# Kernel optimization log

Measured on AMD Instinct MI355X. Metric: run time of the kernel, lower is better.

Reference implementation:

```python
import jax, jax.numpy as jnp
import numpy as np

D_MODEL = 1024
NUM_HEADS = 16
D_K = D_MODEL // NUM_HEADS


def setup_inputs() -> dict:
    key = jax.random.key(0)
    ks = jax.random.split(key, 11)
    B, S = 1, 4096
    s = 1.0 / np.sqrt(D_MODEL)
    return {
        "query": jax.random.normal(ks[0], (B, S, D_MODEL), jnp.float32),
        "key": jax.random.normal(ks[1], (B, S, D_MODEL), jnp.float32),
        "value": jax.random.normal(ks[2], (B, S, D_MODEL), jnp.float32),
        "Wq": jax.random.normal(ks[3], (D_MODEL, D_MODEL), jnp.float32) * s,
        "bq": jnp.zeros((D_MODEL,), jnp.float32),
        "Wk": jax.random.normal(ks[4], (D_MODEL, D_MODEL), jnp.float32) * s,
        "bk": jnp.zeros((D_MODEL,), jnp.float32),
        "Wv": jax.random.normal(ks[5], (D_MODEL, D_MODEL), jnp.float32) * s,
        "bv": jnp.zeros((D_MODEL,), jnp.float32),
        "Wo": jax.random.normal(ks[6], (D_MODEL, D_MODEL), jnp.float32) * s,
        "bo": jnp.zeros((D_MODEL,), jnp.float32),
    }


def reference(query, key, value, Wq, bq, Wk, bk, Wv, bv, Wo, bo):
    B, S, _ = query.shape
    # linear projections, split into heads: [B, H, S, d_k]
    def proj(x, W, b):
        y = x @ W.T + b
        return y.reshape(B, -1, NUM_HEADS, D_K).transpose(0, 2, 1, 3)

    q = proj(query, Wq, bq)
    k = proj(key, Wk, bk)
    v = proj(value, Wv, bv)

    scale = D_K ** (-0.5)
    scores = jnp.einsum("bhqd,bhkd->bhqk", q, k) * scale  # [B,H,S,S]
    attn = jax.nn.softmax(scores, axis=-1)
    out = jnp.einsum("bhqk,bhkd->bhqd", attn, v)  # [B,H,S,d_k]
    out = out.transpose(0, 2, 1, 3).reshape(B, -1, NUM_HEADS * D_K)
    return out @ Wo.T + bo
```

## Files before the change

kernel.cpp:

```cpp
#include <hip/hip_runtime.h>

typedef __bf16 bf16;
typedef __bf16 bf16x8 __attribute__((ext_vector_type(8)));
typedef __bf16 bf16x4 __attribute__((ext_vector_type(4)));
typedef float floatx4 __attribute__((ext_vector_type(4)));

#define MFMA(a, b, c) __builtin_amdgcn_mfma_f32_16x16x32_bf16((a), (b), (c), 0, 0, 0)

__device__ inline bf16x8 load8(const bf16* p) { return *(const bf16x8*)(p); }
__device__ inline bf16x4 load4(const bf16* p) { return *(const bf16x4*)(p); }
__device__ inline bf16x8 cat44(bf16x4 a, bf16x4 b) {
    return __builtin_shufflevector(a, b, 0, 1, 2, 3, 4, 5, 6, 7);
}

__device__ inline void store_c(bf16* p, float v) { *p = (bf16)v; }
__device__ inline void store_c(float* p, float v) { *p = v; }

__device__ inline float fast_exp2(float x) {
#if __has_builtin(__builtin_amdgcn_exp2f)
    return __builtin_amdgcn_exp2f(x);
#else
    float r;
    asm("v_exp_f32 %0, %1" : "=v"(r) : "v"(x));
    return r;
#endif
}

__device__ inline float fast_rcp(float x) {
#if __has_builtin(__builtin_amdgcn_rcpf)
    return __builtin_amdgcn_rcpf(x);
#else
    float r;
    asm("v_rcp_f32 %0, %1" : "=v"(r) : "v"(x));
    return r;
#endif
}

__device__ inline void gload_lds(const bf16* g, bf16* l) {
    __builtin_amdgcn_global_load_lds(
        (const __attribute__((address_space(1))) void*)(g),
        (__attribute__((address_space(3))) void*)(l), 16, 0, 0);
}

struct CvtArgs {
    const float* src[7];
    bf16* dst[7];
    int n[7];
};
__global__ __launch_bounds__(256) void cvt_bf16(CvtArgs a) {
    const int t = blockIdx.y;
    const int i = (blockIdx.x * 256 + threadIdx.x) * 8;
    if (i >= a.n[t]) return;
    const float4 u = *(const float4*)(a.src[t] + i);
    const float4 v = *(const float4*)(a.src[t] + i + 4);
    bf16x8 r;
    r[0] = (bf16)u.x; r[1] = (bf16)u.y; r[2] = (bf16)u.z; r[3] = (bf16)u.w;
    r[4] = (bf16)v.x; r[5] = (bf16)v.y; r[6] = (bf16)v.z; r[7] = (bf16)v.w;
    *(bf16x8*)(a.dst[t] + i) = r;
}

template <typename TC>
__device__ inline void gemm_core(const bf16* __restrict__ A, const bf16* __restrict__ W,
                                 const float* __restrict__ bias, TC* __restrict__ C,
                                 bool TR) {
    __shared__ bf16 As[2][128][32];
    __shared__ bf16 Bs[2][128][32];

    const int tid = threadIdx.x;
    const int wv = tid >> 6, lane = tid & 63;
    const int quad = lane >> 4, lo = lane & 15;
    const int wm = wv >> 1, wn = wv & 1;
    const int Ar0 = blockIdx.y * 128, Br0 = blockIdx.x * 128;

    const int srow = lane >> 2, sseg = (lane & 3) ^ (srow & 3);
    const bf16* Ag = A + (size_t)(Ar0 + srow) * 1024 + sseg * 8;
    const bf16* Bg = W + (size_t)(Br0 + srow) * 1024 + sseg * 8;

    auto stage = [&](int buf, int k0) {
#pragma unroll
        for (int c = 2 * wv; c < 2 * wv + 2; c++) {
            gload_lds(Ag + (size_t)c * 16 * 1024 + k0, &As[buf][c * 16][0]);
            gload_lds(Bg + (size_t)c * 16 * 1024 + k0, &Bs[buf][c * 16][0]);
        }
    };

    floatx4 acc[4][4] = {};
    const int rs = (quad ^ (lo & 3)) * 8;

    stage(0, 0);
    for (int k0 = 0; k0 < 1024; k0 += 32) {
        const int buf = (k0 >> 5) & 1;
        __syncthreads();
        if (k0 + 32 < 1024) stage(buf ^ 1, k0 + 32);

        bf16x8 a[4], b[4];
#pragma unroll
        for (int i = 0; i < 4; i++) a[i] = load8(&As[buf][wm * 64 + i * 16 + lo][rs]);
#pragma unroll
        for (int j = 0; j < 4; j++) b[j] = load8(&Bs[buf][wn * 64 + j * 16 + lo][rs]);
#pragma unroll
        for (int i = 0; i < 4; i++)
#pragma unroll
            for (int j = 0; j < 4; j++) acc[i][j] = MFMA(a[i], b[j], acc[i][j]);
    }

#pragma unroll
    for (int i = 0; i < 4; i++) {
#pragma unroll
        for (int j = 0; j < 4; j++) {
#pragma unroll
            for (int r = 0; r < 4; r++) {
                const int m = Ar0 + wm * 64 + i * 16 + quad * 4 + r;
                const int n = Br0 + wn * 64 + j * 16 + lo;
                const float v = acc[i][j][r] + bias[n];
                if (!TR) {
                    store_c(C + (size_t)m * 1024 + n, v);
                } else {
                    store_c(C + (size_t)(n >> 6) * (64 * 4096) + (size_t)(n & 63) * 4096 + m, v);
                }
            }
        }
    }
}

__global__ __launch_bounds__(256) void gemm_qkv(
    const bf16* __restrict__ qb, const bf16* __restrict__ kb, const bf16* __restrict__ vb,
    const bf16* __restrict__ Wq, const bf16* __restrict__ Wk, const bf16* __restrict__ Wv,
    const float* __restrict__ bq, const float* __restrict__ bk, const float* __restrict__ bv,
    bf16* __restrict__ Q, bf16* __restrict__ Kp, bf16* __restrict__ Vt) {
    if (blockIdx.z == 0)
        gemm_core<bf16>(qb, Wq, bq, Q, false);
    else if (blockIdx.z == 1)
        gemm_core<bf16>(kb, Wk, bk, Kp, false);
    else
        gemm_core<bf16>(vb, Wv, bv, Vt, true);
}

__global__ __launch_bounds__(256) void gemm_o(const bf16* __restrict__ O,
                                              const bf16* __restrict__ Wo,
                                              const float* __restrict__ bo,
                                              float* __restrict__ out) {
    gemm_core<float>(O, Wo, bo, out, false);
}

__global__ __launch_bounds__(256) void flash_attn7(const bf16* __restrict__ Q,
                                                   const bf16* __restrict__ Kmat,
                                                   const bf16* __restrict__ Vt,
                                                   bf16* __restrict__ O) {
    __shared__ bf16 Ks[2][64][64];
    __shared__ bf16 Vs[2][64][64];

    const int tid = threadIdx.x;
    const int wv = tid >> 6;
    const int lane = tid & 63;
    const int quad = lane >> 4, lo = lane & 15;
    const int h = blockIdx.x;
    const int qb = blockIdx.y;
    const int DM = 1024;
    const int q0 = qb * 128 + wv * 32;

    bf16x8 aQ[2][2];
#pragma unroll
    for (int qs = 0; qs < 2; qs++) {
        const bf16* qp = Q + (size_t)(q0 + qs * 16 + lo) * DM + h * 64 + quad * 8;
        aQ[qs][0] = load8(qp);
        aQ[qs][1] = load8(qp + 32);
    }

    bf16x8 bOnes;
#pragma unroll
    for (int i = 0; i < 8; i++) bOnes[i] = (bf16)1.0f;

    floatx4 Oacc[2][4] = {};
    floatx4 Lacc[2] = {};

    const int srow = lane >> 3, sseg = (lane & 7) ^ srow;
    const bf16* Kg = Kmat + (size_t)srow * DM + h * 64 + sseg * 8;
    const bf16* Vg = Vt + (size_t)h * 64 * 4096 + (size_t)srow * 4096 + sseg * 8;

    auto stage = [&](int buf, int kb2) {
#pragma unroll
        for (int c = 2 * wv; c < 2 * wv + 2; c++) {
            gload_lds(Kg + (size_t)(kb2 + c * 8) * DM, &Ks[buf][c * 8][0]);
            gload_lds(Vg + (size_t)(c * 8) * 4096 + kb2, &Vs[buf][c * 8][0]);
        }
    };

    const float C_SCALE = 0.18033688011112043f;
    const float C_BIAS = 23.083120654223415f;
    const int sw = lo & 7;
    const int vo = quad >> 1;
    const int vlo = (quad & 1) * 4;

    stage(0, 0);
    for (int kb2 = 0; kb2 < 4096; kb2 += 64) {
        const int buf = (kb2 >> 6) & 1;
        __syncthreads();
        if (kb2 + 64 < 4096) stage(buf ^ 1, kb2 + 64);

        floatx4 st[2][4];
#pragma unroll
        for (int t = 0; t < 4; t++) {
            const bf16* krow = &Ks[buf][t * 16 + lo][0];
            const bf16x8 aK0 = load8(krow + ((quad ^ sw) * 8));
            const bf16x8 aK1 = load8(krow + (((quad + 4) ^ sw) * 8));
#pragma unroll
            for (int qs = 0; qs < 2; qs++) {
                floatx4 z = {};
                z = MFMA(aK0, aQ[qs][0], z);
                st[qs][t] = MFMA(aK1, aQ[qs][1], z);
            }
        }

        bf16x4 pp[2][4];
#pragma unroll
        for (int qs = 0; qs < 2; qs++)
#pragma unroll
            for (int t = 0; t < 4; t++)
#pragma unroll
                for (int r = 0; r < 4; r++)
                    pp[qs][t][r] = (bf16)fast_exp2(fmaf(st[qs][t][r], C_SCALE, -C_BIAS));

#pragma unroll
        for (int kk = 0; kk < 2; kk++) {
            const bf16x8 aP0 = cat44(pp[0][2 * kk], pp[0][2 * kk + 1]);
            const bf16x8 aP1 = cat44(pp[1][2 * kk], pp[1][2 * kk + 1]);
            Lacc[0] = MFMA(aP0, bOnes, Lacc[0]);
            Lacc[1] = MFMA(aP1, bOnes, Lacc[1]);
#pragma unroll
            for (int nt = 0; nt < 4; nt++) {
                const bf16* vrow = &Vs[buf][nt * 16 + lo][0];
                const bf16x4 v0 = load4(vrow + (((kk * 4 + vo) ^ sw) << 3) + vlo);
                const bf16x4 v1 = load4(vrow + (((kk * 4 + 2 + vo) ^ sw) << 3) + vlo);
                const bf16x8 bV = cat44(v0, v1);
                Oacc[0][nt] = MFMA(aP0, bV, Oacc[0][nt]);
                Oacc[1][nt] = MFMA(aP1, bV, Oacc[1][nt]);
            }
        }
    }

#pragma unroll
    for (int qs = 0; qs < 2; qs++)
#pragma unroll
        for (int r = 0; r < 4; r++) {
            const float inv = fast_rcp(Lacc[qs][r]);
#pragma unroll
            for (int nt = 0; nt < 4; nt++) {
                O[(size_t)(q0 + qs * 16 + quad * 4 + r) * DM + h * 64 + nt * 16 + lo] =
                    (bf16)(Oacc[qs][nt][r] * inv);
            }
        }
}

extern "C" void kernel_launch(void* const* d_in, const int* in_sizes, int n_in,
                              void* d_out, int out_size, void* d_ws, size_t ws_size,
                              hipStream_t stream) {
    const float* query = (const float*)d_in[0];
    const float* key_i = (const float*)d_in[1];
    const float* value = (const float*)d_in[2];
    const float* Wq = (const float*)d_in[3];
    const float* bq = (const float*)d_in[4];
    const float* Wk = (const float*)d_in[5];
    const float* bk = (const float*)d_in[6];
    const float* Wv = (const float*)d_in[7];
    const float* bv = (const float*)d_in[8];
    const float* Wo = (const float*)d_in[9];
    const float* bo = (const float*)d_in[10];

    bf16* ws = (bf16*)d_ws;
    const size_t SZ = (size_t)4096 * 1024;
    const size_t WZ = (size_t)1024 * 1024;
    bf16* qb = ws;
    bf16* kb = ws + SZ;
    bf16* vb = ws + 2 * SZ;
    bf16* Wqb = ws + 3 * SZ;
    bf16* Wkb = ws + 3 * SZ + WZ;
    bf16* Wvb = ws + 3 * SZ + 2 * WZ;
    bf16* Wob = ws + 3 * SZ + 3 * WZ;
    bf16* Q = ws + 3 * SZ + 4 * WZ;
    bf16* K = Q + SZ;
    bf16* Vt = Q + 2 * SZ;
    bf16* O = qb;

    CvtArgs ca;
    const int SZi = 4096 * 1024, WZi = 1024 * 1024;
    ca.src[0] = query; ca.dst[0] = qb;  ca.n[0] = SZi;
    ca.src[1] = key_i; ca.dst[1] = kb;  ca.n[1] = SZi;
    ca.src[2] = value; ca.dst[2] = vb;  ca.n[2] = SZi;
    ca.src[3] = Wq;    ca.dst[3] = Wqb; ca.n[3] = WZi;
    ca.src[4] = Wk;    ca.dst[4] = Wkb; ca.n[4] = WZi;
    ca.src[5] = Wv;    ca.dst[5] = Wvb; ca.n[5] = WZi;
    ca.src[6] = Wo;    ca.dst[6] = Wob; ca.n[6] = WZi;
    cvt_bf16<<<dim3(2048, 7), 256, 0, stream>>>(ca);

    gemm_qkv<<<dim3(8, 32, 3), 256, 0, stream>>>(qb, kb, vb, Wqb, Wkb, Wvb,
                                                 bq, bk, bv, Q, K, Vt);
    flash_attn7<<<dim3(16, 32), 256, 0, stream>>>(Q, K, Vt, O);
    gemm_o<<<dim3(8, 32), 256, 0, stream>>>(O, Wob, bo, (float*)d_out);
}
```

Baseline: 258.5 us.

## Split flash-attention block into eight waves of sixteen query rows each

The attention kernel now launches 512 threads per block, and each of the eight waves handles 16 query rows instead of 32. K/V staging is spread so each wave loads one 8-row chunk. The aim is more waves in flight per CU to hide LDS and exp latency, and lower register pressure per wave. The cost is that each wave reuses every K/V fragment read from LDS for half as many query rows, so LDS traffic per MFMA doubles.

```diff
diff --git a/kernel.cpp b/kernel.cpp
--- a/kernel.cpp
+++ b/kernel.cpp
@@ -143,7 +143,7 @@
     gemm_core<float>(O, Wo, bo, out, false);
 }
 
-__global__ __launch_bounds__(256) void flash_attn7(const bf16* __restrict__ Q,
+__global__ __launch_bounds__(512) void flash_attn8(const bf16* __restrict__ Q,
                                                    const bf16* __restrict__ Kmat,
                                                    const bf16* __restrict__ Vt,
                                                    bf16* __restrict__ O) {
@@ -157,33 +157,29 @@
     const int h = blockIdx.x;
     const int qb = blockIdx.y;
     const int DM = 1024;
-    const int q0 = qb * 128 + wv * 32;
-
-    bf16x8 aQ[2][2];
-#pragma unroll
-    for (int qs = 0; qs < 2; qs++) {
-        const bf16* qp = Q + (size_t)(q0 + qs * 16 + lo) * DM + h * 64 + quad * 8;
-        aQ[qs][0] = load8(qp);
-        aQ[qs][1] = load8(qp + 32);
+    const int q0 = qb * 128 + wv * 16;
+
+    bf16x8 aQ[2];
+    {
+        const bf16* qp = Q + (size_t)(q0 + lo) * DM + h * 64 + quad * 8;
+        aQ[0] = load8(qp);
+        aQ[1] = load8(qp + 32);
     }
 
     bf16x8 bOnes;
 #pragma unroll
     for (int i = 0; i < 8; i++) bOnes[i] = (bf16)1.0f;
 
-    floatx4 Oacc[2][4] = {};
-    floatx4 Lacc[2] = {};
+    floatx4 Oacc[4] = {};
+    floatx4 Lacc = {};
 
     const int srow = lane >> 3, sseg = (lane & 7) ^ srow;
     const bf16* Kg = Kmat + (size_t)srow * DM + h * 64 + sseg * 8;
     const bf16* Vg = Vt + (size_t)h * 64 * 4096 + (size_t)srow * 4096 + sseg * 8;
 
     auto stage = [&](int buf, int kb2) {
-#pragma unroll
-        for (int c = 2 * wv; c < 2 * wv + 2; c++) {
-            gload_lds(Kg + (size_t)(kb2 + c * 8) * DM, &Ks[buf][c * 8][0]);
-            gload_lds(Vg + (size_t)(c * 8) * 4096 + kb2, &Vs[buf][c * 8][0]);
-        }
+        gload_lds(Kg + (size_t)(kb2 + wv * 8) * DM, &Ks[buf][wv * 8][0]);
+        gload_lds(Vg + (size_t)(wv * 8) * 4096 + kb2, &Vs[buf][wv * 8][0]);
     };
 
     const float C_SCALE = 0.18033688011112043f;
@@ -198,58 +194,48 @@
         __syncthreads();
         if (kb2 + 64 < 4096) stage(buf ^ 1, kb2 + 64);
 
-        floatx4 st[2][4];
+        floatx4 st[4];
 #pragma unroll
         for (int t = 0; t < 4; t++) {
             const bf16* krow = &Ks[buf][t * 16 + lo][0];
             const bf16x8 aK0 = load8(krow + ((quad ^ sw) * 8));
             const bf16x8 aK1 = load8(krow + (((quad + 4) ^ sw) * 8));
-#pragma unroll
-            for (int qs = 0; qs < 2; qs++) {
-                floatx4 z = {};
-                z = MFMA(aK0, aQ[qs][0], z);
-                st[qs][t] = MFMA(aK1, aQ[qs][1], z);
-            }
-        }
-
-        bf16x4 pp[2][4];
-#pragma unroll
-        for (int qs = 0; qs < 2; qs++)
-#pragma unroll
-            for (int t = 0; t < 4; t++)
-#pragma unroll
-                for (int r = 0; r < 4; r++)
-                    pp[qs][t][r] = (bf16)fast_exp2(fmaf(st[qs][t][r], C_SCALE, -C_BIAS));
+            floatx4 z = {};
+            z = MFMA(aK0, aQ[0], z);
+            st[t] = MFMA(aK1, aQ[1], z);
+        }
+
+        bf16x4 pp[4];
+#pragma unroll
+        for (int t = 0; t < 4; t++)
+#pragma unroll
+            for (int r = 0; r < 4; r++)
+                pp[t][r] = (bf16)fast_exp2(fmaf(st[t][r], C_SCALE, -C_BIAS));
 
 #pragma unroll
         for (int kk = 0; kk < 2; kk++) {
-            const bf16x8 aP0 = cat44(pp[0][2 * kk], pp[0][2 * kk + 1]);
-            const bf16x8 aP1 = cat44(pp[1][2 * kk], pp[1][2 * kk + 1]);
-            Lacc[0] = MFMA(aP0, bOnes, Lacc[0]);
-            Lacc[1] = MFMA(aP1, bOnes, Lacc[1]);
+            const bf16x8 aP = cat44(pp[2 * kk], pp[2 * kk + 1]);
+            Lacc = MFMA(aP, bOnes, Lacc);
 #pragma unroll
             for (int nt = 0; nt < 4; nt++) {
                 const bf16* vrow = &Vs[buf][nt * 16 + lo][0];
                 const bf16x4 v0 = load4(vrow + (((kk * 4 + vo) ^ sw) << 3) + vlo);
                 const bf16x4 v1 = load4(vrow + (((kk * 4 + 2 + vo) ^ sw) << 3) + vlo);
                 const bf16x8 bV = cat44(v0, v1);
-                Oacc[0][nt] = MFMA(aP0, bV, Oacc[0][nt]);
-                Oacc[1][nt] = MFMA(aP1, bV, Oacc[1][nt]);
+                Oacc[nt] = MFMA(aP, bV, Oacc[nt]);
             }
         }
     }
 
 #pragma unroll
-    for (int qs = 0; qs < 2; qs++)
-#pragma unroll
-        for (int r = 0; r < 4; r++) {
-            const float inv = fast_rcp(Lacc[qs][r]);
-#pragma unroll
-            for (int nt = 0; nt < 4; nt++) {
-                O[(size_t)(q0 + qs * 16 + quad * 4 + r) * DM + h * 64 + nt * 16 + lo] =
-                    (bf16)(Oacc[qs][nt][r] * inv);
-            }
-        }
+    for (int r = 0; r < 4; r++) {
+        const float inv = fast_rcp(Lacc[r]);
+#pragma unroll
+        for (int nt = 0; nt < 4; nt++) {
+            O[(size_t)(q0 + quad * 4 + r) * DM + h * 64 + nt * 16 + lo] =
+                (bf16)(Oacc[nt][r] * inv);
+        }
+    }
 }
 
 extern "C" void kernel_launch(void* const* d_in, const int* in_sizes, int n_in,
@@ -295,6 +281,6 @@
 
     gemm_qkv<<<dim3(8, 32, 3), 256, 0, stream>>>(qb, kb, vb, Wqb, Wkb, Wvb,
                                                  bq, bk, bv, Q, K, Vt);
-    flash_attn7<<<dim3(16, 32), 256, 0, stream>>>(Q, K, Vt, O);
+    flash_attn8<<<dim3(16, 32), 512, 0, stream>>>(Q, K, Vt, O);
     gemm_o<<<dim3(8, 32), 256, 0, stream>>>(O, Wob, bo, (float*)d_out);
 }
```

After: 269.1 us. 4.1% more time.

## Software-pipeline attention: overlap previous tile's PV MFMAs with current exp

Applied to the files above, without the earlier changes.

Restructures the flash attention loop so the P·V matmul for tile i-1 is issued after the QK^T MFMAs of tile i and before the exp of tile i. MFMA work can then overlap the transcendental exp work. V gets a triple-buffered LDS ring so the previous tile's V stays valid while the next one is staged. The cost is extra registers for the carried P fragments and more LDS use.

```diff
diff --git a/kernel.cpp b/kernel.cpp
--- a/kernel.cpp
+++ b/kernel.cpp
@@ -143,12 +143,12 @@
     gemm_core<float>(O, Wo, bo, out, false);
 }
 
-__global__ __launch_bounds__(256) void flash_attn7(const bf16* __restrict__ Q,
+__global__ __launch_bounds__(256) void flash_attn9(const bf16* __restrict__ Q,
                                                    const bf16* __restrict__ Kmat,
                                                    const bf16* __restrict__ Vt,
                                                    bf16* __restrict__ O) {
     __shared__ bf16 Ks[2][64][64];
-    __shared__ bf16 Vs[2][64][64];
+    __shared__ bf16 Vs[3][64][64];
 
     const int tid = threadIdx.x;
     const int wv = tid >> 6;
@@ -178,12 +178,15 @@
     const bf16* Kg = Kmat + (size_t)srow * DM + h * 64 + sseg * 8;
     const bf16* Vg = Vt + (size_t)h * 64 * 4096 + (size_t)srow * 4096 + sseg * 8;
 
-    auto stage = [&](int buf, int kb2) {
-#pragma unroll
-        for (int c = 2 * wv; c < 2 * wv + 2; c++) {
-            gload_lds(Kg + (size_t)(kb2 + c * 8) * DM, &Ks[buf][c * 8][0]);
-            gload_lds(Vg + (size_t)(c * 8) * 4096 + kb2, &Vs[buf][c * 8][0]);
-        }
+    auto stageK = [&](int kb, int kb2) {
+#pragma unroll
+        for (int c = 2 * wv; c < 2 * wv + 2; c++)
+            gload_lds(Kg + (size_t)(kb2 + c * 8) * DM, &Ks[kb][c * 8][0]);
+    };
+    auto stageV = [&](int vb, int kb2) {
+#pragma unroll
+        for (int c = 2 * wv; c < 2 * wv + 2; c++)
+            gload_lds(Vg + (size_t)(c * 8) * 4096 + kb2, &Vs[vb][c * 8][0]);
     };
 
     const float C_SCALE = 0.18033688011112043f;
@@ -192,16 +195,39 @@
     const int vo = quad >> 1;
     const int vlo = (quad & 1) * 4;
 
-    stage(0, 0);
-    for (int kb2 = 0; kb2 < 4096; kb2 += 64) {
-        const int buf = (kb2 >> 6) & 1;
+    bf16x8 aPrev[2][2];
+
+    auto pv = [&](int vb) {
+#pragma unroll
+        for (int kk = 0; kk < 2; kk++) {
+            Lacc[0] = MFMA(aPrev[0][kk], bOnes, Lacc[0]);
+            Lacc[1] = MFMA(aPrev[1][kk], bOnes, Lacc[1]);
+#pragma unroll
+            for (int nt = 0; nt < 4; nt++) {
+                const bf16* vrow = &Vs[vb][nt * 16 + lo][0];
+                const bf16x4 v0 = load4(vrow + (((kk * 4 + vo) ^ sw) << 3) + vlo);
+                const bf16x4 v1 = load4(vrow + (((kk * 4 + 2 + vo) ^ sw) << 3) + vlo);
+                const bf16x8 bV = cat44(v0, v1);
+                Oacc[0][nt] = MFMA(aPrev[0][kk], bV, Oacc[0][nt]);
+                Oacc[1][nt] = MFMA(aPrev[1][kk], bV, Oacc[1][nt]);
+            }
+        }
+    };
+
+    stageK(0, 0);
+    stageV(0, 0);
+    for (int i = 0; i < 64; i++) {
+        const int kbuf = i & 1;
         __syncthreads();
-        if (kb2 + 64 < 4096) stage(buf ^ 1, kb2 + 64);
+        if (i + 1 < 64) {
+            stageK(kbuf ^ 1, (i + 1) * 64);
+            stageV((i + 1) % 3, (i + 1) * 64);
+        }
 
         floatx4 st[2][4];
 #pragma unroll
         for (int t = 0; t < 4; t++) {
-            const bf16* krow = &Ks[buf][t * 16 + lo][0];
+            const bf16* krow = &Ks[kbuf][t * 16 + lo][0];
             const bf16x8 aK0 = load8(krow + ((quad ^ sw) * 8));
             const bf16x8 aK1 = load8(krow + (((quad + 4) ^ sw) * 8));
 #pragma unroll
@@ -212,6 +238,8 @@
             }
         }
 
+        if (i > 0) pv((i + 2) % 3);
+
         bf16x4 pp[2][4];
 #pragma unroll
         for (int qs = 0; qs < 2; qs++)
@@ -220,24 +248,13 @@
 #pragma unroll
                 for (int r = 0; r < 4; r++)
                     pp[qs][t][r] = (bf16)fast_exp2(fmaf(st[qs][t][r], C_SCALE, -C_BIAS));
-
-#pragma unroll
-        for (int kk = 0; kk < 2; kk++) {
-            const bf16x8 aP0 = cat44(pp[0][2 * kk], pp[0][2 * kk + 1]);
-            const bf16x8 aP1 = cat44(pp[1][2 * kk], pp[1][2 * kk + 1]);
-            Lacc[0] = MFMA(aP0, bOnes, Lacc[0]);
-            Lacc[1] = MFMA(aP1, bOnes, Lacc[1]);
-#pragma unroll
-            for (int nt = 0; nt < 4; nt++) {
-                const bf16* vrow = &Vs[buf][nt * 16 + lo][0];
-                const bf16x4 v0 = load4(vrow + (((kk * 4 + vo) ^ sw) << 3) + vlo);
-                const bf16x4 v1 = load4(vrow + (((kk * 4 + 2 + vo) ^ sw) << 3) + vlo);
-                const bf16x8 bV = cat44(v0, v1);
-                Oacc[0][nt] = MFMA(aP0, bV, Oacc[0][nt]);
-                Oacc[1][nt] = MFMA(aP1, bV, Oacc[1][nt]);
-            }
-        }
+#pragma unroll
+        for (int qs = 0; qs < 2; qs++)
+#pragma unroll
+            for (int kk = 0; kk < 2; kk++)
+                aPrev[qs][kk] = cat44(pp[qs][2 * kk], pp[qs][2 * kk + 1]);
     }
+    pv(63 % 3);
 
 #pragma unroll
     for (int qs = 0; qs < 2; qs++)
@@ -295,6 +312,6 @@
 
     gemm_qkv<<<dim3(8, 32, 3), 256, 0, stream>>>(qb, kb, vb, Wqb, Wkb, Wvb,
                                                  bq, bk, bv, Q, K, Vt);
-    flash_attn7<<<dim3(16, 32), 256, 0, stream>>>(Q, K, Vt, O);
+    flash_attn9<<<dim3(16, 32), 256, 0, stream>>>(Q, K, Vt, O);
     gemm_o<<<dim3(8, 32), 256, 0, stream>>>(O, Wob, bo, (float*)d_out);
 }
```

New measurement: 279.5 us. +8.1%, slower.
